# Kernel tuning notes

Measured on AMD Instinct MI355X. Metric: run time of the kernel, lower is better.

Reference implementation:

```python
import jax, jax.numpy as jnp
from jax import lax
import numpy as np


def setup_inputs() -> dict:
    key = jax.random.key(0)
    k1, k2, k3, k4 = jax.random.split(key, 4)
    B, L, T = 8192, 48, 49  # batch of sentence pairs, len_A, extended_length_B+1
    emissions = jax.random.normal(k1, (B, L, T), dtype=jnp.float32)
    trans_feats = jax.random.normal(k2, (T, T, 6), dtype=jnp.float32)
    w2 = jax.random.normal(k3, (6,), dtype=jnp.float32)
    b2 = jax.random.normal(k4, (1,), dtype=jnp.float32)
    return {"emissions": emissions, "trans_feats": trans_feats, "w2": w2, "b2": b2}


def reference(emissions, trans_feats, w2, b2):
    """Batched CRF forward algorithm (_forward_alg with max_span_size=1).

    emissions:   [B, len_A, T]  word-pair interaction scores (output_both)
    trans_feats: [T, T, 6]      6-dim transition features; mlp2 maps -> scalar
    Returns alpha (log partition) per batch element, shape [B].
    """
    B, L, T = emissions.shape
    # mlp2: Linear(6, 1). trans[j, k] = score of transitioning from state k to j.
    trans = jnp.einsum('jkf,f->jk', trans_feats, w2) + b2[0]
    # Original indexes feat[j-1]: state j uses emission column (j-1) mod T.
    emit = jnp.roll(emissions, 1, axis=2)  # [B, L, T]
    # i == 0: forward_var starts at 0, no transition; logsumexp over the
    # broadcast emit score adds log(T).
    f0 = emit[:, 0, :] + jnp.log(jnp.asarray(T, dtype=emissions.dtype))  # [B, T]

    def step(f, e_i):
        # f: [B, T] previous forward vars; next[b, j] = lse_k(f[b,k] + trans[j,k]) + e_i[b,j]
        nf = jax.nn.logsumexp(f[:, None, :] + trans[None, :, :], axis=2) + e_i
        return nf, None

    fL, _ = lax.scan(step, f0, jnp.moveaxis(emit[:, 1:, :], 1, 0))  # scan over len_A-1 steps
    alpha = jax.nn.logsumexp(fL, axis=1)  # [B]
    return alpha
```

## Files before the change

### kernel.cpp

```cpp
#include <hip/hip_runtime.h>
#include <math.h>

#define TS 49
#define LOG49 3.8918202981106265f
#define LN2 0.6931471805599453f

typedef short bf16x8 __attribute__((ext_vector_type(8)));
typedef float f32x4 __attribute__((ext_vector_type(4)));
typedef float f32x4u __attribute__((ext_vector_type(4), aligned(4)));


__global__ void prep_kernel(const float* __restrict__ tf, const float* __restrict__ w2,
                            const float* __restrict__ b2, float* __restrict__ ws) {
    __shared__ float tr[TS * TS];
    __shared__ float red[256];
    const int tid = threadIdx.x;
    const float w0 = w2[0], w1 = w2[1], w2v = w2[2], w3 = w2[3], w4 = w2[4], w5 = w2[5];
    const float bb = b2[0];
    float lmax = -INFINITY;
    for (int idx = tid; idx < TS * TS; idx += 256) {
        const float* p = tf + idx * 6;
        float s = bb + p[0]*w0 + p[1]*w1 + p[2]*w2v + p[3]*w3 + p[4]*w4 + p[5]*w5;
        tr[idx] = s;
        lmax = fmaxf(lmax, s);
    }
    red[tid] = lmax;
    __syncthreads();
    for (int s = 128; s > 0; s >>= 1) {
        if (tid < s) red[tid] = fmaxf(red[tid], red[tid + s]);
        __syncthreads();
    }
    const float Tmax = red[0];
    __syncthreads();
    unsigned short* B = (unsigned short*)ws;
    for (int idx = tid; idx < 4096; idx += 256) {
        const int s  = idx & 7;
        const int l  = (idx >> 3) & 63;
        const int h  = (idx >> 9) & 1;
        const int nt = idx >> 10;
        const int jp = 4 * (l & 15) + nt;
        const int kp = 32 * h + 8 * (l >> 4) + s;
        float v = 0.0f;
        if (jp < TS && kp < TS) {
            const int jj = (jp + 1) % TS, kk = (kp + 1) % TS;
            v = __expf(tr[jj * TS + kk] - Tmax);
        }
        unsigned bts = __float_as_uint(v);
        B[idx] = (unsigned short)((bts + 0x7FFFu + ((bts >> 16) & 1u)) >> 16);
    }
    if (tid == 0) ((float*)ws)[2048] = Tmax;
}

__device__ __forceinline__ unsigned cvtpk_bf16(float lo, float hi) {
    unsigned d;
    asm("v_cvt_pk_bf16_f32 %0, %1, %2" : "=v"(d) : "v"(lo), "v"(hi));
    return d;
}

__global__ __launch_bounds__(64, 2) void crf_fwd(const float* __restrict__ emis,
                                                 const unsigned short* __restrict__ wsB,
                                                 float* __restrict__ out, int L) {
    __shared__ __align__(16) unsigned short V16[1024];
    const int l = threadIdx.x, g = l >> 4, c0 = l & 15;
    const int b0 = blockIdx.x * 4;
    const float Tmax = ((const float*)wsB)[2048];

    bf16x8 Bf[4][2];
    {
        const bf16x8* Bt = (const bf16x8*)wsB;
        #pragma unroll
        for (int nt = 0; nt < 4; ++nt)
            #pragma unroll
            for (int h = 0; h < 2; ++h) Bf[nt][h] = Bt[(nt * 2 + h) * 64 + l];
    }

    int wi[4];
    #pragma unroll
    for (int t = 0; t < 4; ++t) {
        const int ch = 4 * g + t;
        wi[t] = ch * 16 + (c0 ^ ((ch & 7) << 1));
    }
    const int ra0 = c0 * 8 + (g ^ (c0 & 7));
    const int ra1 = c0 * 8 + ((4 + g) ^ (c0 & 7));
    uint2* const Vw = (uint2*)V16;
    const bf16x8* const Vr = (const bf16x8*)V16;

    {
        const uint2 z = {0u, 0u};
        Vw[wi[1]] = z;
        Vw[wi[2]] = z;
        Vw[wi[3]] = z;
    }

    const int LT = L * TS;
    const bool sel12 = (c0 >= 12);
    const int col4 = sel12 ? 45 : 4 * c0;
    const float* const ebase = emis + (size_t)(b0 + g) * LT + col4;

    f32x4 pf[4];

#define LQ(STEP, SLOT) do {                                                           \
    pf[SLOT] = *(const f32x4u*)(ebase + (STEP) * TS);                                 \
} while (0)

#define EESEL(DST, SLOT) do {                                                         \
    const f32x4 q = pf[SLOT];                                                         \
    DST[0] = __expf(sel12 ? q.w : q.x);                                               \
    DST[1] = __expf(q.y);                                                             \
    DST[2] = __expf(q.z);                                                             \
    DST[3] = __expf(q.w);                                                             \
} while (0)

    LQ(0, 0);
    if (L > 1) LQ(1, 1);
    if (L > 2) LQ(2, 2);
    if (L > 3) LQ(3, 3);

    float v[4];
    {
        const f32x4 q = pf[0];
        const float i0 = sel12 ? q.w : q.x;
        v[0] = (4 * c0 + 0 < TS) ? __expf(i0)  : 0.0f;
        v[1] = (4 * c0 + 1 < TS) ? __expf(q.y) : 0.0f;
        v[2] = (4 * c0 + 2 < TS) ? __expf(q.z) : 0.0f;
        v[3] = (4 * c0 + 3 < TS) ? __expf(q.w) : 0.0f;
    }

    float ee0[4], ee1[4];
    EESEL(ee1, 1);

    float sc = 0.f, fac = 1.f, pend = 0.f;

#define STEP(I, EC, EN, SN, SL, DO_C, DO_A) do {                                      \
                          \
    {                                                                                 \
        uint2 u;                                                                      \
        u.x = cvtpk_bf16(v[0], v[1]);                                                 \
        u.y = cvtpk_bf16(v[2], v[3]);                                                 \
        Vw[wi[0]] = u;                                                                \
    }                                                                                 \
                   \
    EESEL(EN, SN);                                                                    \
                                 \
    if ((I) + 3 < L) LQ((I) + 3, SL);                                                 \
    asm volatile("" ::: "memory");                                                    \
                      \
    const bf16x8 A0 = Vr[ra0];                                                        \
    const bf16x8 A1 = Vr[ra1];                                                        \
                           \
    _Pragma("unroll")                                                                 \
    for (int nt = 0; nt < 4; ++nt) {                                                  \
        f32x4 acc = {0.f, 0.f, 0.f, 0.f};                                             \
        acc = __builtin_amdgcn_mfma_f32_16x16x32_bf16(A0, Bf[nt][0], acc, 0, 0, 0);   \
        acc = __builtin_amdgcn_mfma_f32_16x16x32_bf16(A1, Bf[nt][1], acc, 0, 0, 0);   \
        float nv = acc[0] * EC[nt];                                                   \
        if (DO_A) nv *= fac;                                                          \
        v[nt] = nv;                                                                   \
    }                                                                                 \
    if (DO_A) sc += pend;                                                             \
                         \
    if (DO_C) {                                                                       \
        float mx = fmaxf(fmaxf(v[0], v[1]), fmaxf(v[2], v[3]));                       \
        mx = fmaxf(mx, __shfl_xor(mx, 1, 64));                                        \
        mx = fmaxf(mx, __shfl_xor(mx, 2, 64));                                        \
        mx = fmaxf(mx, __shfl_xor(mx, 4, 64));                                        \
        mx = fmaxf(mx, __shfl_xor(mx, 8, 64));                                        \
        const unsigned ex = __float_as_uint(mx) >> 23;                                \
        fac  = __uint_as_float((254u - ex) << 23);                                    \
        pend = (float)((int)ex - 127) * LN2;                                          \
    }                                                                                 \
} while (0)

    const int S = L - 1;
    int i = 1;
    for (; i + 3 <= S; i += 4) {
        STEP(i + 0, ee1, ee0, 2, 0, 1, 0);
        STEP(i + 1, ee0, ee1, 3, 1, 0, 1);
        STEP(i + 2, ee1, ee0, 0, 2, 0, 0);
        STEP(i + 3, ee0, ee1, 1, 3, 0, 0);
    }
    if (i <= S)     STEP(i,     ee1, ee0, 2, 0, 1, 0);
    if (i + 1 <= S) STEP(i + 1, ee0, ee1, 3, 1, 0, 1);
    if (i + 2 <= S) STEP(i + 2, ee1, ee0, 0, 2, 0, 0);
#undef STEP
#undef EESEL
#undef LQ

    float s = (v[0] + v[1]) + (v[2] + v[3]);
    s += __shfl_xor(s, 1, 64);
    s += __shfl_xor(s, 2, 64);
    s += __shfl_xor(s, 4, 64);
    s += __shfl_xor(s, 8, 64);
    const float res = sc + __logf(s) + LOG49 + (float)(L - 1) * Tmax;
    if (c0 == 0) out[b0 + g] = res;
}

extern "C" void kernel_launch(void* const* d_in, const int* in_sizes, int n_in,
                              void* d_out, int out_size, void* d_ws, size_t ws_size,
                              hipStream_t stream) {
    const float* emis = (const float*)d_in[0];
    const float* tf   = (const float*)d_in[1];
    const float* w2   = (const float*)d_in[2];
    const float* b2   = (const float*)d_in[3];
    float* out = (float*)d_out;
    float* ws  = (float*)d_ws;

    const int B = out_size;
    const int L = in_sizes[0] / (B * TS);

    prep_kernel<<<1, 256, 0, stream>>>(tf, w2, b2, ws);
    crf_fwd<<<B / 4, 64, 0, stream>>>(emis, (const unsigned short*)ws, out, L);
}
```

Baseline: 28.60 us.

## Stream emissions through LDS via global_load_lds with deeper prefetch

Replaces the register-held float4 emission prefetch with direct global-to-LDS loads into an 8-slot ring buffer, prefetching 5 steps ahead and gating each step with explicit vmcnt waits. Launch bounds raise the occupancy hint from 2 to 4 blocks per CU, and the unroll pattern changes so renormalization runs every two steps instead of every four. The aim is to hide global load latency better and free registers, at the cost of extra LDS traffic and hand-counted waitcnt values. Rescaling every two steps also adds reduction work and changes how much the values can drift between rescales.

```diff
diff --git a/kernel.cpp b/kernel.cpp
--- a/kernel.cpp
+++ b/kernel.cpp
@@ -7,7 +7,6 @@
 
 typedef short bf16x8 __attribute__((ext_vector_type(8)));
 typedef float f32x4 __attribute__((ext_vector_type(4)));
-typedef float f32x4u __attribute__((ext_vector_type(4), aligned(4)));
 
 
 __global__ void prep_kernel(const float* __restrict__ tf, const float* __restrict__ w2,
@@ -57,10 +56,11 @@
     return d;
 }
 
-__global__ __launch_bounds__(64, 2) void crf_fwd(const float* __restrict__ emis,
+__global__ __launch_bounds__(64, 4) void crf_fwd(const float* __restrict__ emis,
                                                  const unsigned short* __restrict__ wsB,
                                                  float* __restrict__ out, int L) {
     __shared__ __align__(16) unsigned short V16[1024];
+    __shared__ __align__(16) float EMIS[2048];
     const int l = threadIdx.x, g = l >> 4, c0 = l & 15;
     const int b0 = blockIdx.x * 4;
     const float Tmax = ((const float*)wsB)[2048];
@@ -95,43 +95,57 @@
     const int LT = L * TS;
     const bool sel12 = (c0 >= 12);
     const int col4 = sel12 ? 45 : 4 * c0;
-    const float* const ebase = emis + (size_t)(b0 + g) * LT + col4;
-
-    f32x4 pf[4];
-
-#define LQ(STEP, SLOT) do {                                                           \
-    pf[SLOT] = *(const f32x4u*)(ebase + (STEP) * TS);                                 \
+    const float* const eb = emis + (size_t)(b0 + g) * LT + col4;
+
+#define GLL(STEP_) do {                                                               \
+    const float* _s = eb + (STEP_) * TS;                                              \
+    float* _d = &EMIS[((STEP_) & 7) << 8];                                            \
+    _Pragma("unroll")                                                                 \
+    for (int j = 0; j < 4; ++j)                                                       \
+        __builtin_amdgcn_global_load_lds(                                             \
+            (const __attribute__((address_space(1))) void*)(_s + j),                  \
+            (__attribute__((address_space(3))) void*)(_d + j * 64), 4, 0, 0);         \
 } while (0)
 
-#define EESEL(DST, SLOT) do {                                                         \
-    const f32x4 q = pf[SLOT];                                                         \
-    DST[0] = __expf(sel12 ? q.w : q.x);                                               \
-    DST[1] = __expf(q.y);                                                             \
-    DST[2] = __expf(q.z);                                                             \
-    DST[3] = __expf(q.w);                                                             \
+#define EESEL(DST, STEP_) do {                                                        \
+    const float* _p = &EMIS[((STEP_) & 7) << 8];                                      \
+    const float q0 = _p[l];                                                           \
+    const float q1 = _p[64 + l];                                                      \
+    const float q2 = _p[128 + l];                                                     \
+    const float q3 = _p[192 + l];                                                     \
+    DST[0] = __expf(sel12 ? q3 : q0);                                                 \
+    DST[1] = __expf(q1);                                                              \
+    DST[2] = __expf(q2);                                                              \
+    DST[3] = __expf(q3);                                                              \
 } while (0)
 
-    LQ(0, 0);
-    if (L > 1) LQ(1, 1);
-    if (L > 2) LQ(2, 2);
-    if (L > 3) LQ(3, 3);
+    GLL(0);
+    if (L > 1) GLL(1);
+    if (L > 2) GLL(2);
+    if (L > 3) GLL(3);
+    if (L > 4) GLL(4);
+    if (L > 5) GLL(5);
 
     float v[4];
+    asm volatile("s_waitcnt vmcnt(20)" ::: "memory");
     {
-        const f32x4 q = pf[0];
-        const float i0 = sel12 ? q.w : q.x;
-        v[0] = (4 * c0 + 0 < TS) ? __expf(i0)  : 0.0f;
-        v[1] = (4 * c0 + 1 < TS) ? __expf(q.y) : 0.0f;
-        v[2] = (4 * c0 + 2 < TS) ? __expf(q.z) : 0.0f;
-        v[3] = (4 * c0 + 3 < TS) ? __expf(q.w) : 0.0f;
-    }
-
+        const float* _p = &EMIS[0];
+        const float q0 = _p[l], q1 = _p[64 + l], q2 = _p[128 + l], q3 = _p[192 + l];
+        const float i0 = sel12 ? q3 : q0;
+        v[0] = (4 * c0 + 0 < TS) ? __expf(i0) : 0.0f;
+        v[1] = (4 * c0 + 1 < TS) ? __expf(q1) : 0.0f;
+        v[2] = (4 * c0 + 2 < TS) ? __expf(q2) : 0.0f;
+        v[3] = (4 * c0 + 3 < TS) ? __expf(q3) : 0.0f;
+    }
     float ee0[4], ee1[4];
+    asm volatile("s_waitcnt vmcnt(16)" ::: "memory");
     EESEL(ee1, 1);
 
     float sc = 0.f, fac = 1.f, pend = 0.f;
 
-#define STEP(I, EC, EN, SN, SL, DO_C, DO_A) do {                                      \
+#define STEP(I, EC, EN, DO_C, DO_A) do {                                              \
+                    \
+    if ((I) + 5 < L) GLL((I) + 5);                                                    \
                           \
     {                                                                                 \
         uint2 u;                                                                      \
@@ -139,15 +153,14 @@
         u.y = cvtpk_bf16(v[2], v[3]);                                                 \
         Vw[wi[0]] = u;                                                                \
     }                                                                                 \
-                   \
-    EESEL(EN, SN);                                                                    \
-                                 \
-    if ((I) + 3 < L) LQ((I) + 3, SL);                                                 \
-    asm volatile("" ::: "memory");                                                    \
+           \
+    asm volatile("s_waitcnt vmcnt(16)" ::: "memory");                                 \
+                                                      \
+    EESEL(EN, (I) + 1);                                                               \
                       \
     const bf16x8 A0 = Vr[ra0];                                                        \
     const bf16x8 A1 = Vr[ra1];                                                        \
-                           \
+                             \
     _Pragma("unroll")                                                                 \
     for (int nt = 0; nt < 4; ++nt) {                                                  \
         f32x4 acc = {0.f, 0.f, 0.f, 0.f};                                             \
@@ -173,18 +186,14 @@
 
     const int S = L - 1;
     int i = 1;
-    for (; i + 3 <= S; i += 4) {
-        STEP(i + 0, ee1, ee0, 2, 0, 1, 0);
-        STEP(i + 1, ee0, ee1, 3, 1, 0, 1);
-        STEP(i + 2, ee1, ee0, 0, 2, 0, 0);
-        STEP(i + 3, ee0, ee1, 1, 3, 0, 0);
-    }
-    if (i <= S)     STEP(i,     ee1, ee0, 2, 0, 1, 0);
-    if (i + 1 <= S) STEP(i + 1, ee0, ee1, 3, 1, 0, 1);
-    if (i + 2 <= S) STEP(i + 2, ee1, ee0, 0, 2, 0, 0);
+    for (; i + 1 <= S; i += 2) {
+        STEP(i + 0, ee1, ee0, 1, 0);
+        STEP(i + 1, ee0, ee1, 0, 1);
+    }
+    if (i <= S) STEP(i, ee1, ee0, 0, 0);
 #undef STEP
 #undef EESEL
-#undef LQ
+#undef GLL
 
     float s = (v[0] + v[1]) + (v[2] + v[3]);
     s += __shfl_xor(s, 1, 64);
```

Result: slower. 41.63 us (+45.6%).
